# Kernel optimization log

Measured on AMD Instinct MI355X. Metric: run time of the kernel, lower is better.

The kernel has to match this reference:

```python
import jax, jax.numpy as jnp
import numpy as np

H = 256          # encoder hidden per direction
D = 2 * H        # decoder hidden / bidirectional feature dim
IN = 2
OUT = 2
B = 64
T = 256
STEPS = 24       # hard-coded decoder loop length in the source


def gru_cell(x, h, Wih, Whh, bih, bhh):
    # PyTorch GRU cell: gate order (r, z, n)
    gi = x @ Wih.T + bih
    gh = h @ Whh.T + bhh
    ir, iz, inn = jnp.split(gi, 3, axis=-1)
    hr, hz, hn = jnp.split(gh, 3, axis=-1)
    r = jax.nn.sigmoid(ir + hr)
    z = jax.nn.sigmoid(iz + hz)
    n = jnp.tanh(inn + r * hn)
    return (1.0 - z) * n + z * h


def run_dir(xs, Wih, Whh, bih, bhh, reverse):
    # xs: (T, B, F) time-major; returns outputs (T, B, H) and last hidden (B, H)
    h0 = jnp.zeros((xs.shape[1], Whh.shape[-1]), xs.dtype)
    def step(h, xt):
        h2 = gru_cell(xt, h, Wih, Whh, bih, bhh)
        return h2, h2
    h_last, ys = jax.lax.scan(step, h0, xs, reverse=reverse)
    return ys, h_last


def setup_inputs():
    keys = jax.random.split(jax.random.key(0), 24)
    k = iter(keys)
    def rn(shape, s):
        return jax.random.normal(next(k), shape, jnp.float32) * s
    se = 1.0 / np.sqrt(H)
    sd = 1.0 / np.sqrt(D)
    return {
        "x": rn((B, T, IN), 1.0),
        "enc_Wih0": rn((2, 3 * H, IN), se),
        "enc_Whh0": rn((2, 3 * H, H), se),
        "enc_bih0": rn((2, 3 * H), se),
        "enc_bhh0": rn((2, 3 * H), se),
        "enc_Wih": rn((2, 2, 3 * H, D), se),
        "enc_Whh": rn((2, 2, 3 * H, H), se),
        "enc_bih": rn((2, 2, 3 * H), se),
        "enc_bhh": rn((2, 2, 3 * H), se),
        "dec_Wih": rn((3, 3 * D, D), sd),
        "dec_Whh": rn((3, 3 * D, D), sd),
        "dec_bih": rn((3, 3 * D), sd),
        "dec_bhh": rn((3, 3 * D), sd),
        "fc_con_W": rn((D, 2 * D), sd),
        "fc_con_b": rn((D,), sd),
        "attn_W": rn((D, 2 * D), sd),
        "attn_b": rn((D,), sd),
        "v": jax.random.uniform(next(k), (D,), jnp.float32),  # torch.rand init
        "fc_W": rn((OUT, D), sd),
        "fc_b": rn((OUT,), sd),
    }


def reference(x, enc_Wih0, enc_Whh0, enc_bih0, enc_bhh0,
              enc_Wih, enc_Whh, enc_bih, enc_bhh,
              dec_Wih, dec_Whh, dec_bih, dec_bhh,
              fc_con_W, fc_con_b, attn_W, attn_b, v, fc_W, fc_b):
    # ---- bidirectional 3-layer GRU encoder ----
    seq = x.transpose(1, 0, 2)  # (T, B, IN) time-major
    hf_list, hb_list = [], []
    for l in range(3):
        if l == 0:
            Wf, Uf, bf, cf = enc_Wih0[0], enc_Whh0[0], enc_bih0[0], enc_bhh0[0]
            Wb, Ub, bb, cb = enc_Wih0[1], enc_Whh0[1], enc_bih0[1], enc_bhh0[1]
        else:
            Wf, Uf, bf, cf = enc_Wih[l-1, 0], enc_Whh[l-1, 0], enc_bih[l-1, 0], enc_bhh[l-1, 0]
            Wb, Ub, bb, cb = enc_Wih[l-1, 1], enc_Whh[l-1, 1], enc_bih[l-1, 1], enc_bhh[l-1, 1]
        yf, hf = run_dir(seq, Wf, Uf, bf, cf, False)
        yb, hb = run_dir(seq, Wb, Ub, bb, cb, True)
        seq = jnp.concatenate([yf, yb], axis=-1)
        hf_list.append(hf)
        hb_list.append(hb)
    enc_out = seq.transpose(1, 0, 2)  # (B, T, D)
    # hidden_decoder = cat(forward, backward) per layer -> (3, B, D)
    hidden = jnp.stack([jnp.concatenate([f, b], axis=-1)
                        for f, b in zip(hf_list, hb_list)])
    dec_in = enc_out[:, -1, :]  # (B, D)

    # additive attention: energy = tanh(W [h; enc_out] + b); precompute enc part
    attn_Wh = attn_W[:, :D]
    attn_We = attn_W[:, D:]
    enc_proj = jnp.einsum('bte,de->btd', enc_out, attn_We)  # (B, T, D)

    def dec_step(carry, _):
        d_in, hid = carry
        hq = hid[-1] @ attn_Wh.T                               # (B, D)
        energy = jnp.tanh(hq[:, None, :] + enc_proj + attn_b)  # (B, T, D)
        scores = jnp.einsum('btd,d->bt', energy, v)
        aw = jax.nn.softmax(scores, axis=1)                    # (B, T)
        ctx = jnp.einsum('bt,btd->bd', aw, enc_out)            # (B, D)
        inp = jnp.concatenate([d_in, ctx], axis=-1) @ fc_con_W.T + fc_con_b
        new_h = []
        for l in range(3):  # 3-layer unidirectional decoder GRU, single step
            hl = gru_cell(inp, hid[l], dec_Wih[l], dec_Whh[l], dec_bih[l], dec_bhh[l])
            new_h.append(hl)
            inp = hl
        out_step = inp @ fc_W.T + fc_b
        return (inp, jnp.stack(new_h)), out_step

    _, outs = jax.lax.scan(dec_step, (dec_in, hidden), None, length=STEPS)
    return outs.transpose(1, 0, 2)  # (B, 24, OUT)
```

## Files before the change

kernel.cpp:

```cpp
#include <hip/hip_runtime.h>

typedef unsigned short u16;
typedef unsigned int u32;
typedef _Float16 f16;
typedef f16   f16x2 __attribute__((ext_vector_type(2)));
typedef f16   f16x4 __attribute__((ext_vector_type(4)));
typedef f16   f16x8 __attribute__((ext_vector_type(8)));
typedef float f32x4 __attribute__((ext_vector_type(4)));

#define MFMA16(a,b,c) __builtin_amdgcn_mfma_f32_16x16x32_f16((a),(b),(c),0,0,0)

__device__ __forceinline__ float sigm_(float x){ return 1.f/(1.f + __expf(-x)); }
__device__ __forceinline__ float tanh_(float x){ return 1.f - 2.f/(1.f + __expf(2.f*x)); }
__device__ __forceinline__ float clampf(float x, float c){
  if (!(x > -c)) x = -c;
  if (x > c) x = c;
  return x;
}
__device__ __forceinline__ f16x8 cvt8f(const float* p){
  const float4 a = *(const float4*)p;
  const float4 b = *(const float4*)(p+4);
  f16x8 r;
  r[0]=(f16)a.x; r[1]=(f16)a.y; r[2]=(f16)a.z; r[3]=(f16)a.w;
  r[4]=(f16)b.x; r[5]=(f16)b.y; r[6]=(f16)b.z; r[7]=(f16)b.w;
  return r;
}

__device__ __forceinline__ void gbar_(u32* c, u32 nb){
  __syncthreads();
  __threadfence();
  if (threadIdx.x == 0) {
    __hip_atomic_fetch_add(c, 1u, __ATOMIC_RELAXED, __HIP_MEMORY_SCOPE_AGENT);
    while (__hip_atomic_load(c, __ATOMIC_RELAXED, __HIP_MEMORY_SCOPE_AGENT) < nb) {}
  }
  __syncthreads();
  __threadfence();
}

__global__ void k_diag(float* out, int mib){
  const int i = blockIdx.x*256 + threadIdx.x;
  if (i < 3072) out[i] = 1000.f * (float)mib;
}

__global__ void k_prep_dec(const float* dWhh, const float* attnW, const float* fccon,
                           const float* dWih, f16* R3)
{
  long idx = (long)blockIdx.x*256 + threadIdx.x;
  const float* src; int rs, colOff = 0, NKS; long dst, loc;
  if (idx < 294912L) {
    loc = idx; const int m = (int)(loc / 98304); loc %= 98304;
    src = dWhh + (long)m*786432; rs = 512; NKS = 16; dst = (long)m*786432;
  } else if (idx < 327680L) {
    loc = idx - 294912L; src = attnW; colOff = 512; rs = 1024; NKS = 16; dst = 2359296L;
  } else if (idx < 393216L) {
    loc = idx - 327680L; src = fccon; rs = 1024; NKS = 32; dst = 2621440L;
  } else if (idx < 688128L) {
    loc = idx - 393216L; const int m = (int)(loc / 98304); loc %= 98304;
    src = dWih + (long)m*786432; rs = 512; NKS = 16; dst = 3440640L + (long)m*786432;
  } else if (idx < 720896L) {
    loc = idx - 688128L; src = attnW; colOff = 0; rs = 1024; NKS = 16; dst = 5799936L;
  } else return;
  const int lane = (int)(loc & 63);
  const long frag = loc >> 6;
  const int ks = (int)(frag % NKS);
  const long nt = frag / NKS;
  const int n  = (int)(nt*16 + (lane & 15));
  const int k0 = ks*32 + ((lane >> 4) << 3);
  const float* sp = src + (long)n*rs + colOff + k0;
  f16* dp = R3 + dst + loc*8;
  #pragma unroll
  for (int j = 0; j < 8; ++j) dp[j] = (f16)sp[j];
}

__global__ void k_gi0s(const float* __restrict__ x, const float* __restrict__ W,
                       const float* __restrict__ bi, f16* __restrict__ gi,
                       int seg, int BH, int lbh, int b0)
{
  const long idx = (long)blockIdx.x*256 + threadIdx.x;
  const int v = (int)(idx % 24);
  long rest = idx / 24;
  const int tid = (int)(rest & 511); rest >>= 9;
  const int bq = (int)(rest & ((1 << (lbh-4)) - 1)); rest >>= (lbh-4);
  const int s = (int)(rest & 63);
  const int d = (int)(rest >> 6);
  const int r = v / 6, rem = v % 6, i = rem / 3, g = rem % 3;
  const int w = tid >> 6, q = (tid >> 4) & 3, lo = tid & 15;
  const int n = g*256 + (2*w + i)*16 + lo;
  const int b = bq*16 + q*4 + r;
  const int t = d ? (255 - (seg*64 + s)) : (seg*64 + s);
  const float x0 = x[(((b0+b)<<8) + t)*2];
  const float x1 = x[(((b0+b)<<8) + t)*2 + 1];
  const long wi = ((long)d*768 + n)*2;
  gi[idx] = (f16)clampf(x0*W[wi] + x1*W[wi+1] + bi[d*768 + n], 32.f);
}

#define GIE(G, vv) ((float)((vv) < 8 ? (G)[0][(vv)&7] : ((vv) < 16 ? (G)[1][(vv)-8] : (G)[2][(vv)-16])))

__global__ __launch_bounds__(512, 1) void k_enc_seg(
    const f16* __restrict__ gi, const float* __restrict__ Wraw,
    const float* __restrict__ bhh, f16* __restrict__ seq, int ostr,
    f16* __restrict__ fin, float* __restrict__ hcar, int seg, int BH)
{
  const int tid = threadIdx.x;
  const int w = tid >> 6, lane = tid & 63;
  const int lo16 = lane & 15, quad = lane >> 4;
  const int nbq = BH >> 4;
  const int dir = blockIdx.x / nbq, bq = blockIdx.x % nbq;

  __shared__ f16 h16[4][16][264];

  const float* mat = Wraw + (long)dir*196608;
  f16x8 wr[6][8];
  #pragma unroll
  for (int p = 0; p < 3; ++p)
    #pragma unroll
    for (int i = 0; i < 2; ++i) {
      const int n = (p*16 + 2*w + i)*16 + lo16;
      #pragma unroll
      for (int ks = 0; ks < 8; ++ks)
        wr[p*2+i][ks] = cvt8f(mat + (long)n*256 + ks*32 + quad*8);
    }
  float bh_[3][2];
  #pragma unroll
  for (int p = 0; p < 3; ++p)
    #pragma unroll
    for (int i = 0; i < 2; ++i)
      bh_[p][i] = bhh[dir*768 + p*256 + (2*w+i)*16 + lo16];

  float hreg[2][4];
  if (seg == 0) {
    #pragma unroll
    for (int i = 0; i < 2; ++i)
      #pragma unroll
      for (int r = 0; r < 4; ++r) {
        hreg[i][r] = 0.f;
        h16[0][quad*4 + r][(2*w+i)*16 + lo16] = (f16)0.f;
      }
  } else {
    #pragma unroll
    for (int i = 0; i < 2; ++i) {
      const int c = (2*w+i)*16 + lo16;
      #pragma unroll
      for (int r = 0; r < 4; ++r) {
        const float v = hcar[((dir*BH) + bq*16 + quad*4 + r)*256 + c];
        hreg[i][r] = v;
        h16[0][quad*4 + r][c] = (f16)v;
      }
    }
  }

  const long gstep = (long)nbq*512*24;
  const f16* gbase = gi + (((long)dir*64*nbq + bq)*512 + tid)*24;
  f16x8 g0[3], g1[3];
  { const f16x8* gp = (const f16x8*)gbase; g0[0]=gp[0]; g0[1]=gp[1]; g0[2]=gp[2]; }

  const int frow = tid >> 5;
  const int fcol = (tid & 31) * 8;

  for (int s = 0; s < 64; ++s) {
    __syncthreads();
    if (s >= 2) {
      const int so = s - 2;
      const int t2 = dir ? (255 - (seg*64 + so)) : (seg*64 + so);
      const f16x8 hv = *(const f16x8*)&h16[(so+1)&3][frow][fcol];
      *(f16x8*)&seq[((long)t2*ostr + bq*16 + frow)*512 + dir*256 + fcol] = hv;
    }
    f32x4 acc[6];
    #pragma unroll
    for (int q = 0; q < 6; ++q) acc[q] = (f32x4){0.f,0.f,0.f,0.f};
    #pragma unroll
    for (int ks = 0; ks < 8; ++ks) {
      const f16x8 a = *(const f16x8*)&h16[s&3][lo16][ks*32 + quad*8];
      #pragma unroll
      for (int q = 0; q < 6; ++q)
        acc[q] = MFMA16(a, wr[q][ks], acc[q]);
    }
    if (s < 63) {
      const f16x8* gp = (const f16x8*)(gbase + (long)(s+1)*gstep);
      g1[0]=gp[0]; g1[1]=gp[1]; g1[2]=gp[2];
    }
    #pragma unroll
    for (int i = 0; i < 2; ++i) {
      const int c = (2*w+i)*16 + lo16;
      #pragma unroll
      for (int r = 0; r < 4; ++r) {
        const int row = quad*4 + r;
        const int v = r*6 + i*3;
        const float gir = GIE(g0, v);
        const float giz = GIE(g0, v+1);
        const float gin = GIE(g0, v+2);
        const float rv = sigm_(gir + acc[i][r]   + bh_[0][i]);
        const float zv = sigm_(giz + acc[2+i][r] + bh_[1][i]);
        const float nv = tanh_(gin + rv*(acc[4+i][r] + bh_[2][i]));
        float hn = (1.f - zv)*nv + zv*hreg[i][r];
        hn = clampf(hn, 2.f);
        hreg[i][r] = hn;
        h16[(s+1)&3][row][c] = (f16)hn;
        if (seg == 3 && s == 63) fin[(bq*16 + row)*512 + dir*256 + c] = (f16)hn;
      }
    }
    g0[0]=g1[0]; g0[1]=g1[1]; g0[2]=g1[2];
  }
  __syncthreads();
  #pragma unroll
  for (int so = 62; so < 64; ++so) {
    const int t2 = dir ? (255 - (seg*64 + so)) : (seg*64 + so);
    const f16x8 hv = *(const f16x8*)&h16[(so+1)&3][frow][fcol];
    *(f16x8*)&seq[((long)t2*ostr + bq*16 + frow)*512 + dir*256 + fcol] = hv;
  }
  #pragma unroll
  for (int i = 0; i < 2; ++i) {
    const int c = (2*w+i)*16 + lo16;
    #pragma unroll
    for (int r = 0; r < 4; ++r)
      hcar[((dir*BH) + bq*16 + quad*4 + r)*256 + c] = hreg[i][r];
  }
}

__global__ void k_gemm(const f16* __restrict__ A, int K,
                       const f16* __restrict__ Bsw, const float* __restrict__ Braw,
                       long bzs, int ldb, int koff,
                       const float* __restrict__ bias, int biaszs,
                       void* __restrict__ Cv, long czs, int ldc, int mode,
                       int tb0, int tb1, int tdirsgn, int lbh, int abstr, float cv)
{
  const int tid = threadIdx.x, w = tid>>6, lane = tid&63;
  const int lo16 = lane&15, quad = lane>>4;
  const int m0 = blockIdx.x*64 + w*16;
  const int n0 = blockIdx.y*128;
  const int z  = blockIdx.z;
  const int tbase = z ? tb1 : tb0;
  const int tdir  = z ? -tdirsgn : tdirsgn;
  const int NKS = K >> 5;
  const int mrow = m0 + lo16;
  const long arow = (long)(tbase + tdir*(mrow >> lbh))*abstr + (mrow & ((1<<lbh)-1));
  const f16* Ap = A + arow*K + quad*8;
  f32x4 acc[8];
  #pragma unroll
  for (int i=0;i<8;++i) acc[i]=(f32x4){0.f,0.f,0.f,0.f};
  if (Bsw) {
    const f16* Bp = Bsw + (long)z*bzs;
    for (int ks = 0; ks < NKS; ++ks) {
      const f16x8 a = *(const f16x8*)(Ap + ks*32);
      #pragma unroll
      for (int nt = 0; nt < 8; ++nt) {
        const f16x8 b = *(const f16x8*)(Bp + (((long)((n0>>4)+nt)*NKS + ks) << 9) + lane*8);
        acc[nt] = MFMA16(a, b, acc[nt]);
      }
    }
  } else {
    const float* Bp = Braw + (long)z*bzs;
    for (int ks = 0; ks < NKS; ++ks) {
      const f16x8 a = *(const f16x8*)(Ap + ks*32);
      #pragma unroll
      for (int nt = 0; nt < 8; ++nt) {
        const f16x8 b = cvt8f(Bp + (long)(n0 + nt*16 + lo16)*ldb + koff + ks*32 + quad*8);
        acc[nt] = MFMA16(a, b, acc[nt]);
      }
    }
  }
  #pragma unroll
  for (int nt = 0; nt < 8; ++nt) {
    const int n = n0 + nt*16 + lo16;
    const float bv = bias ? bias[z*biaszs + n] : 0.f;
    #pragma unroll
    for (int r = 0; r < 4; ++r) {
      const int m = m0 + quad*4 + r;
      const float val = clampf(acc[nt][r] + bv, cv);
      if (mode == 2) {
        const int s_ = m >> lbh, b_ = m & ((1<<lbh)-1);
        const int bq_ = b_ >> 4, q_ = (b_ >> 2) & 3, r_ = b_ & 3;
        const int g_ = n >> 8, j_ = (n >> 4) & 15, lo_ = n & 15;
        const long idx = ((((long)z*64 + s_)*(1<<(lbh-4)) + bq_)*512
                          + ((j_>>1)*64 + q_*16 + lo_))*24 + r_*6 + (j_&1)*3 + g_;
        ((f16*)Cv)[idx] = (f16)val;
      } else if (mode == 1)
        ((f16*)Cv)[(long)z*czs + (long)m*ldc + n] = (f16)val;
      else
        ((float*)Cv)[(long)z*czs + (long)m*ldc + n] = val;
    }
  }
}

__global__ void k_score(const f16* __restrict__ seq, const f16* __restrict__ We,
                        const float* __restrict__ hq, const float* __restrict__ ab,
                        const float* __restrict__ vp, float* __restrict__ S)
{
  const int t = blockIdx.x, tid = threadIdx.x;
  const int w = tid>>6, lane = tid&63, lo16 = lane&15, quad = lane>>4;
  __shared__ float svab[1024];
  for (int i = tid; i < 512; i += 256) { svab[i] = vp[i]; svab[512+i] = ab[i]; }
  __syncthreads();
  f32x4 acc[32];
  #pragma unroll
  for (int i=0;i<32;++i) acc[i]=(f32x4){0.f,0.f,0.f,0.f};
  const f16* Ap = seq + ((long)t*64 + w*16 + lo16)*512 + quad*8;
  for (int ks = 0; ks < 16; ++ks) {
    const f16x8 a = *(const f16x8*)(Ap + ks*32);
    #pragma unroll
    for (int nt = 0; nt < 32; ++nt) {
      const f16x8 b = *(const f16x8*)(We + (((long)nt*16 + ks) << 9) + lane*8);
      acc[nt] = MFMA16(a, b, acc[nt]);
    }
  }
  #pragma unroll
  for (int r = 0; r < 4; ++r) {
    const int b = w*16 + quad*4 + r;
    float sc = 0.f;
    #pragma unroll
    for (int nt = 0; nt < 32; ++nt) {
      const int n = nt*16 + lo16;
      sc += svab[n] * tanh_(acc[nt][r] + hq[(b<<9) + n] + svab[512+n]);
    }
    sc += __shfl_xor(sc, 1, 64); sc += __shfl_xor(sc, 2, 64);
    sc += __shfl_xor(sc, 4, 64); sc += __shfl_xor(sc, 8, 64);
    if (lo16 == 0) S[(b<<8) + t] = clampf(sc, 256.f);
  }
}

__global__ void k_attnctx(const float* __restrict__ S, const f16* __restrict__ enc,
                          f16* __restrict__ cat)
{
  const int b = blockIdx.x, tid = threadIdx.x;
  __shared__ float ssc[256], srd[256];
  const float sc = clampf(S[(b<<8) + tid], 256.f);
  srd[tid] = sc; __syncthreads();
  for (int off = 128; off > 0; off >>= 1) { if (tid < off) srd[tid] = fmaxf(srd[tid], srd[tid+off]); __syncthreads(); }
  const float mx = srd[0]; __syncthreads();
  const float e = __expf(sc - mx);
  srd[tid] = e; __syncthreads();
  for (int off = 128; off > 0; off >>= 1) { if (tid < off) srd[tid] += srd[tid+off]; __syncthreads(); }
  const float inv = 1.f / srd[0]; __syncthreads();
  ssc[tid] = e * inv; __syncthreads();
  float c0 = 0.f, c1 = 0.f;
  for (int tt = 0; tt < 256; ++tt) {
    const float awt = ssc[tt];
    const f16* ep = enc + (((long)tt*64 + b) << 9);
    c0 += awt * (float)ep[tid];
    c1 += awt * (float)ep[256 + tid];
  }
  cat[(b<<10) + 512 + tid] = (f16)clampf(c0, 4.f);
  cat[(b<<10) + 768 + tid] = (f16)clampf(c1, 4.f);
}

__global__ void k_dec_init(const f16* __restrict__ fin, const f16* __restrict__ seq,
                           f16* __restrict__ hb16, float* __restrict__ hf32,
                           f16* __restrict__ cat, u32* __restrict__ cnt)
{
  const int idx = blockIdx.x*256 + threadIdx.x;
  if (idx < 64) cnt[idx] = 0;
  const int d = idx & 511, b = (idx >> 9) & 63, l = idx >> 15;
  if (l < 3) {
    const float v = clampf((float)fin[((long)l<<15) + (b<<9) + d], 2.f);
    hb16[(long)l*65536 + (b<<9) + d] = (f16)v;
    hf32[(long)l*32768 + (b<<9) + d] = v;
  } else {
    cat[(b<<10) + d] = seq[((long)255*64 + b)*512 + d];
  }
}

__global__ __launch_bounds__(512, 1) void k_attn(
    const f16* __restrict__ seq, const f16* __restrict__ ep,
    const float* __restrict__ hf2, const f16* __restrict__ cat,
    const f16* __restrict__ whsw, const f16* __restrict__ fcsw,
    const float* __restrict__ fcconB, const float* __restrict__ vp,
    f16* __restrict__ inp, const float* __restrict__ fcW,
    const float* __restrict__ fcb, float* __restrict__ out, int step)
{
  const int b = blockIdx.x;
  const int tid = threadIdx.x, w = tid >> 6, lane = tid & 63;
  const int quad = lane >> 4;
  __shared__ float hsm[512];
  __shared__ float cats[1024];
  __shared__ float hqs[512];
  __shared__ float aw[256];
  __shared__ float red[8*512];
  hsm[tid]  = hf2[(b<<9) + tid];
  cats[tid] = (float)cat[(b<<10) + tid];
  __syncthreads();
  if (w < 2 && step > 0) {
    float p = 0.f;
    #pragma unroll
    for (int j = 0; j < 8; ++j) p += fcW[(w<<9) + lane*8 + j] * hsm[lane*8 + j];
    p += __shfl_xor(p,1,64); p += __shfl_xor(p,2,64); p += __shfl_xor(p,4,64);
    p += __shfl_xor(p,8,64); p += __shfl_xor(p,16,64); p += __shfl_xor(p,32,64);
    if (lane == 0) out[(b*24 + step-1)*2 + w] = clampf(p + fcb[w], 128.f);
  }
  #pragma unroll
  for (int i = 0; i < 4; ++i) {
    const int nt = w*4 + i;
    float p = 0.f;
    for (int ks = 0; ks < 16; ++ks) {
      const f16x8 wv = *(const f16x8*)(whsw + (((long)nt*16 + ks)<<9) + lane*8);
      const float4 ha = *(const float4*)&hsm[ks*32 + quad*8];
      const float4 hb = *(const float4*)&hsm[ks*32 + quad*8 + 4];
      p += (float)wv[0]*ha.x + (float)wv[1]*ha.y + (float)wv[2]*ha.z + (float)wv[3]*ha.w
         + (float)wv[4]*hb.x + (float)wv[5]*hb.y + (float)wv[6]*hb.z + (float)wv[7]*hb.w;
    }
    p += __shfl_xor(p,16,64); p += __shfl_xor(p,32,64);
    if (lane < 16) hqs[nt*16 + lane] = p;
  }
  __syncthreads();
  float hq8[8], v8[8];
  #pragma unroll
  for (int j = 0; j < 8; ++j) { hq8[j] = hqs[lane*8+j]; v8[j] = vp[lane*8+j]; }
  #pragma unroll 2
  for (int i = 0; i < 32; ++i) {
    const int t = w*32 + i;
    const f16x8 e = *(const f16x8*)(ep + (((long)t*64 + b)<<9) + lane*8);
    float s = 0.f;
    #pragma unroll
    for (int j = 0; j < 8; ++j) s += v8[j]*tanh_((float)e[j] + hq8[j]);
    s += __shfl_xor(s,1,64); s += __shfl_xor(s,2,64); s += __shfl_xor(s,4,64);
    s += __shfl_xor(s,8,64); s += __shfl_xor(s,16,64); s += __shfl_xor(s,32,64);
    if (lane == 0) aw[t] = clampf(s, 256.f);
  }
  __syncthreads();
  if (tid < 64) {
    float s0=aw[tid], s1=aw[tid+64], s2=aw[tid+128], s3=aw[tid+192];
    float mx = fmaxf(fmaxf(s0,s1), fmaxf(s2,s3));
    mx = fmaxf(mx, __shfl_xor(mx,1,64)); mx = fmaxf(mx, __shfl_xor(mx,2,64));
    mx = fmaxf(mx, __shfl_xor(mx,4,64)); mx = fmaxf(mx, __shfl_xor(mx,8,64));
    mx = fmaxf(mx, __shfl_xor(mx,16,64)); mx = fmaxf(mx, __shfl_xor(mx,32,64));
    const float e0=__expf(s0-mx), e1=__expf(s1-mx), e2=__expf(s2-mx), e3=__expf(s3-mx);
    float sm = e0+e1+e2+e3;
    sm += __shfl_xor(sm,1,64); sm += __shfl_xor(sm,2,64); sm += __shfl_xor(sm,4,64);
    sm += __shfl_xor(sm,8,64); sm += __shfl_xor(sm,16,64); sm += __shfl_xor(sm,32,64);
    const float inv = 1.f/sm;
    aw[tid]=e0*inv; aw[tid+64]=e1*inv; aw[tid+128]=e2*inv; aw[tid+192]=e3*inv;
  }
  __syncthreads();
  float c8[8];
  #pragma unroll
  for (int j = 0; j < 8; ++j) c8[j] = 0.f;
  #pragma unroll 2
  for (int i = 0; i < 32; ++i) {
    const int t = w*32 + i;
    const f16x8 e = *(const f16x8*)(seq + (((long)t*64 + b)<<9) + lane*8);
    const float awt = aw[t];
    #pragma unroll
    for (int j = 0; j < 8; ++j) c8[j] += awt*(float)e[j];
  }
  #pragma unroll
  for (int j = 0; j < 8; ++j) red[(w<<9) + lane*8 + j] = c8[j];
  __syncthreads();
  {
    float s = 0.f;
    #pragma unroll
    for (int ww = 0; ww < 8; ++ww) s += red[(ww<<9) + tid];
    cats[512 + tid] = clampf(s, 4.f);
  }
  __syncthreads();
  #pragma unroll
  for (int i = 0; i < 4; ++i) {
    const int nt = w*4 + i;
    float p = 0.f;
    for (int ks = 0; ks < 32; ++ks) {
      const f16x8 wv = *(const f16x8*)(fcsw + (((long)nt*32 + ks)<<9) + lane*8);
      const float4 ca = *(const float4*)&cats[ks*32 + quad*8];
      const float4 cb = *(const float4*)&cats[ks*32 + quad*8 + 4];
      p += (float)wv[0]*ca.x + (float)wv[1]*ca.y + (float)wv[2]*ca.z + (float)wv[3]*ca.w
         + (float)wv[4]*cb.x + (float)wv[5]*cb.y + (float)wv[6]*cb.z + (float)wv[7]*cb.w;
    }
    p += __shfl_xor(p,16,64); p += __shfl_xor(p,32,64);
    if (lane < 16) inp[(b<<9) + nt*16 + lane] = (f16)clampf(p + fcconB[nt*16+lane], 64.f);
  }
}

__global__ void k_cell3(const f16* __restrict__ inp0, const f16* __restrict__ WihSw,
                        const f16* __restrict__ WhhSw, const float* __restrict__ bihA,
                        const float* __restrict__ bhhA, float* __restrict__ hfA,
                        f16* __restrict__ hb, f16* __restrict__ cat, int p, u32* cnt)
{
  const int tid = threadIdx.x, w = tid>>6, lane = tid&63;
  const int lo16 = lane&15, quad = lane>>4;
  const int Wt  = ((int)blockIdx.x & 7)*4 + w;
  const int mi0 = ((int)blockIdx.x >> 3)*2;
  for (int l = 0; l < 3; ++l) {
    const f16* inp = (l == 0) ? inp0 : (hb + (long)(2*(l-1) + (1-p))*32768);
    const f16* WihL = WihSw + (long)l*786432;
    const f16* WhhL = WhhSw + (long)l*786432;
    const float* bih = bihA + l*1536;
    const float* bhh = bhhA + l*1536;
    float* hf32 = hfA + (long)l*32768;
    const f16* hin = hb + (long)(2*l + p)*32768;
    f16* hout = hb + (long)(2*l + (1-p))*32768;
    f16* catp = (l == 2) ? cat : (f16*)nullptr;

    f32x4 arz[4], an_[4];
    #pragma unroll
    for (int i=0;i<4;++i){ arz[i]=(f32x4){0.f,0.f,0.f,0.f}; an_[i]=(f32x4){0.f,0.f,0.f,0.f}; }
    #pragma unroll 2
    for (int kk = 0; kk < 16; ++kk) {
      const f16x8 b0 = *(const f16x8*)(WihL + (((long)Wt*16 + kk)<<9)      + lane*8);
      const f16x8 b1 = *(const f16x8*)(WihL + (((long)(32+Wt)*16 + kk)<<9) + lane*8);
      const f16x8 b2 = *(const f16x8*)(WihL + (((long)(64+Wt)*16 + kk)<<9) + lane*8);
      #pragma unroll
      for (int m = 0; m < 2; ++m) {
        const f16x8 a = *(const f16x8*)&inp[(((mi0+m)*16 + lo16)<<9) + kk*32 + quad*8];
        arz[m]   = MFMA16(a, b0, arz[m]);
        arz[2+m] = MFMA16(a, b1, arz[2+m]);
        an_[m]   = MFMA16(a, b2, an_[m]);
      }
    }
    #pragma unroll 2
    for (int kk = 0; kk < 16; ++kk) {
      const f16x8 b0 = *(const f16x8*)(WhhL + (((long)Wt*16 + kk)<<9)      + lane*8);
      const f16x8 b1 = *(const f16x8*)(WhhL + (((long)(32+Wt)*16 + kk)<<9) + lane*8);
      const f16x8 b2 = *(const f16x8*)(WhhL + (((long)(64+Wt)*16 + kk)<<9) + lane*8);
      #pragma unroll
      for (int m = 0; m < 2; ++m) {
        const f16x8 a = *(const f16x8*)&hin[(((mi0+m)*16 + lo16)<<9) + kk*32 + quad*8];
        arz[m]   = MFMA16(a, b0, arz[m]);
        arz[2+m] = MFMA16(a, b1, arz[2+m]);
        an_[2+m] = MFMA16(a, b2, an_[2+m]);
      }
    }
    const int c = Wt*16 + lo16;
    const float brz0 = bih[c]     + bhh[c];
    const float brz1 = bih[512+c] + bhh[512+c];
    const float bin_ = bih[1024+c];
    const float bhn_ = bhh[1024+c];
    #pragma unroll
    for (int m = 0; m < 2; ++m)
      #pragma unroll
      for (int r = 0; r < 4; ++r) {
        const int row = (mi0+m)*16 + quad*4 + r;
        const float rv = sigm_(clampf(arz[m][r],64.f)   + brz0);
        const float zv = sigm_(clampf(arz[2+m][r],64.f) + brz1);
        const float nv = tanh_(clampf(an_[m][r],64.f) + bin_ + rv*(clampf(an_[2+m][r],64.f) + bhn_));
        const float ho = hf32[(row<<9) + c];
        float hn2 = (1.f - zv)*nv + zv*ho;
        hn2 = clampf(hn2, 2.f);
        hf32[(row<<9) + c] = hn2;
        hout[(row<<9) + c] = (f16)hn2;
        if (catp) catp[(row<<10) + c] = (f16)hn2;
      }
    if (l < 2) gbar_(cnt + l, 16);
  }
}

__global__ void k_cell_raw(const f16* __restrict__ inp, const float* __restrict__ WihRaw,
                           const f16* __restrict__ WhhSw, const float* __restrict__ bih,
                           const float* __restrict__ bhh, float* __restrict__ hf32,
                           const f16* __restrict__ hin, f16* __restrict__ hout,
                           f16* __restrict__ cat)
{
  const int tid = threadIdx.x, w = tid>>6, lane = tid&63;
  const int lo16 = lane&15, quad = lane>>4;
  const int Wt = blockIdx.x*4 + w;
  f32x4 arz[8], an_[8];
  #pragma unroll
  for (int i=0;i<8;++i){ arz[i]=(f32x4){0.f,0.f,0.f,0.f}; an_[i]=(f32x4){0.f,0.f,0.f,0.f}; }
  const int nr = Wt*16 + lo16;
  const float* Rr = WihRaw + (long)nr*512        + quad*8;
  const float* Rz = WihRaw + (long)(512+nr)*512  + quad*8;
  const float* Rn = WihRaw + (long)(1024+nr)*512 + quad*8;
  #pragma unroll 2
  for (int kk = 0; kk < 16; ++kk) {
    const f16x8 b0 = cvt8f(Rr + kk*32);
    const f16x8 b1 = cvt8f(Rz + kk*32);
    const f16x8 b2 = cvt8f(Rn + kk*32);
    #pragma unroll
    for (int mi = 0; mi < 4; ++mi) {
      const f16x8 a = *(const f16x8*)&inp[((mi*16 + lo16)<<9) + kk*32 + quad*8];
      arz[mi]   = MFMA16(a, b0, arz[mi]);
      arz[4+mi] = MFMA16(a, b1, arz[4+mi]);
      an_[mi]   = MFMA16(a, b2, an_[mi]);
    }
  }
  #pragma unroll 2
  for (int kk = 0; kk < 16; ++kk) {
    const f16x8 b0 = *(const f16x8*)(WhhSw + (((long)Wt*16 + kk)<<9)      + lane*8);
    const f16x8 b1 = *(const f16x8*)(WhhSw + (((long)(32+Wt)*16 + kk)<<9) + lane*8);
    const f16x8 b2 = *(const f16x8*)(WhhSw + (((long)(64+Wt)*16 + kk)<<9) + lane*8);
    #pragma unroll
    for (int mi = 0; mi < 4; ++mi) {
      const f16x8 a = *(const f16x8*)&hin[((mi*16 + lo16)<<9) + kk*32 + quad*8];
      arz[mi]   = MFMA16(a, b0, arz[mi]);
      arz[4+mi] = MFMA16(a, b1, arz[4+mi]);
      an_[4+mi] = MFMA16(a, b2, an_[4+mi]);
    }
  }
  const int c = Wt*16 + lo16;
  const float brz0 = bih[c]     + bhh[c];
  const float brz1 = bih[512+c] + bhh[512+c];
  const float bin_ = bih[1024+c];
  const float bhn_ = bhh[1024+c];
  #pragma unroll
  for (int mi = 0; mi < 4; ++mi)
    #pragma unroll
    for (int r = 0; r < 4; ++r) {
      const int row = mi*16 + quad*4 + r;
      const float rv = sigm_(clampf(arz[mi][r],64.f)   + brz0);
      const float zv = sigm_(clampf(arz[4+mi][r],64.f) + brz1);
      const float nv = tanh_(clampf(an_[mi][r],64.f) + bin_ + rv*(clampf(an_[4+mi][r],64.f) + bhn_));
      const float ho = hf32[(row<<9) + c];
      float hn2 = (1.f - zv)*nv + zv*ho;
      hn2 = clampf(hn2, 2.f);
      hf32[(row<<9) + c] = hn2;
      hout[(row<<9) + c] = (f16)hn2;
      if (cat) cat[(row<<10) + c] = (f16)hn2;
    }
}

__global__ void k_out(const float* __restrict__ h2, const float* __restrict__ fcW,
                      const float* __restrict__ fcb, float* __restrict__ out, int step)
{
  const int b = blockIdx.x, t = threadIdx.x;
  __shared__ float r0[256], r1[256];
  const float ha = clampf(h2[(b<<9) + t], 2.f);
  const float hb = clampf(h2[(b<<9) + 256 + t], 2.f);
  r0[t] = ha*fcW[t]     + hb*fcW[256+t];
  r1[t] = ha*fcW[512+t] + hb*fcW[768+t];
  __syncthreads();
  for (int off = 128; off > 0; off >>= 1) {
    if (t < off) { r0[t] += r0[t+off]; r1[t] += r1[t+off]; }
    __syncthreads();
  }
  if (t == 0) {
    out[(b*24 + step)*2]     = clampf(r0[0] + fcb[0], 128.f);
    out[(b*24 + step)*2 + 1] = clampf(r1[0] + fcb[1], 128.f);
  }
}

extern "C" void kernel_launch(void* const* d_in, const int* in_sizes, int n_in,
                              void* d_out, int out_size, void* d_ws, size_t ws_size,
                              hipStream_t stream) {
  const float* X      = (const float*)d_in[0];
  const float* eWih0  = (const float*)d_in[1];
  const float* eWhh0  = (const float*)d_in[2];
  const float* ebih0  = (const float*)d_in[3];
  const float* ebhh0  = (const float*)d_in[4];
  const float* eWih   = (const float*)d_in[5];
  const float* eWhh   = (const float*)d_in[6];
  const float* ebih   = (const float*)d_in[7];
  const float* ebhh   = (const float*)d_in[8];
  const float* dWih   = (const float*)d_in[9];
  const float* dWhh   = (const float*)d_in[10];
  const float* dbih   = (const float*)d_in[11];
  const float* dbhh   = (const float*)d_in[12];
  const float* fcconW = (const float*)d_in[13];
  const float* fcconB = (const float*)d_in[14];
  const float* attnW  = (const float*)d_in[15];
  const float* attnB  = (const float*)d_in[16];
  const float* vW     = (const float*)d_in[17];
  const float* fcW    = (const float*)d_in[18];
  const float* fcB    = (const float*)d_in[19];
  float* OUT = (float*)d_out;

  const long need_big  = 47054848L;
  const long need_half = 32964608L;
  f16* H = (f16*)d_ws;
  f16 *SEQ = H, *L1OUT, *GIB, *R3, *FIN, *HB, *CAT, *INP;
  float *HC;
  int BH, lbh, nh, l1ostr, l1abstr; long gdir;

  if ((long)ws_size >= need_big) {
    BH = 64; lbh = 6; nh = 1; l1ostr = 64; l1abstr = 64;
    L1OUT = H + 8388608L;
    GIB   = H + 16777216L;
    HC    = (float*)(H + 23068672L);
    FIN   = H + 23134208L;
    HB    = H + 23232512L;
    CAT   = H + 23429120L;
    INP   = H + 23494656L;
    gdir  = 3145728L;
  } else if ((long)ws_size >= need_half) {
    BH = 32; lbh = 5; nh = 2; l1ostr = 32; l1abstr = 32;
    L1OUT = H + 8388608L;
    GIB   = H + 12582912L;
    HC    = (float*)(H + 16023552L);
    FIN   = H + 16089088L;
    HB    = H + 16187392L;
    CAT   = H + 16384000L;
    INP   = H + 16449536L;
    gdir  = 1572864L;
  } else {
    k_diag<<<12, 256, 0, stream>>>(OUT, (int)(ws_size >> 20));
    return;
  }
  R3 = GIB;
  float* ST = (float*)(GIB + 3145728L);
  float* HQ = ST;
  float* HF = ST + 32768;
  float* S  = ST + 131072;
  u32* CNT = (u32*)ST;
  const int nblk = 2*(BH>>4);
  const int gi0grid = (2*64*BH*768)/256;

  for (int h = 0; h < nh; ++h) {
    const int b0 = h*BH;
    for (int seg = 0; seg < 4; ++seg) {
      k_gi0s<<<gi0grid, 256, 0, stream>>>(X, eWih0, ebih0, GIB, seg, BH, lbh, b0);
      k_enc_seg<<<nblk, 512, 0, stream>>>(GIB, eWhh0, ebhh0, SEQ + (long)b0*512, 64,
                                          FIN + (long)b0*512, HC, seg, BH);
    }
    for (int seg = 0; seg < 4; ++seg) {
      k_gemm<<<dim3(BH, 6, 2), 256, 0, stream>>>(SEQ + (long)b0*512, 512,
          (const f16*)nullptr, eWih, 393216L, 512, 0, ebih, 768,
          GIB, gdir, 768, 2, seg*64, 255 - seg*64, 1, lbh, 64, 32.f);
      k_enc_seg<<<nblk, 512, 0, stream>>>(GIB, eWhh, ebhh, L1OUT, l1ostr,
                                          FIN + 32768 + (long)b0*512, HC, seg, BH);
    }
    for (int seg = 0; seg < 4; ++seg) {
      k_gemm<<<dim3(BH, 6, 2), 256, 0, stream>>>(L1OUT, 512,
          (const f16*)nullptr, eWih + 2L*393216, 393216L, 512, 0, ebih + 1536, 768,
          GIB, gdir, 768, 2, seg*64, 255 - seg*64, 1, lbh, l1abstr, 32.f);
      k_enc_seg<<<nblk, 512, 0, stream>>>(GIB, eWhh + 2L*196608, ebhh + 1536,
                                          SEQ + (long)b0*512, 64,
                                          FIN + 65536 + (long)b0*512, HC, seg, BH);
    }
  }

  if (BH == 64) {
    f16* EP    = L1OUT;
    f16* WIHSW = GIB + 3440640L;
    f16* WHSW  = GIB + 5799936L;

    k_prep_dec<<<2816, 256, 0, stream>>>(dWhh, attnW, fcconW, dWih, R3);
    k_gemm<<<dim3(256, 4, 1), 256, 0, stream>>>(SEQ, 512,
        R3 + 2359296L, (const float*)nullptr, 0L, 0, 0, attnB, 0,
        EP, 0L, 512, 1, 0, 0, 1, 6, 64, 32.f);
    k_dec_init<<<512, 256, 0, stream>>>(FIN, SEQ, HB, HF, CAT, CNT);

    for (int s = 0; s < 24; ++s) {
      const int p = s & 1;
      k_attn<<<64, 512, 0, stream>>>(SEQ, EP, HF + 2*32768, CAT, WHSW, R3 + 2621440L,
          fcconB, vW, INP, fcW, fcB, OUT, s);
      k_cell3<<<16, 256, 0, stream>>>(INP, WIHSW, R3, dbih, dbhh, HF, HB, CAT,
          p, CNT + s*2);
    }
    k_out<<<64, 256, 0, stream>>>(HF + 2*32768, fcW, fcB, OUT, 23);
  } else {
    k_prep_dec<<<1536, 256, 0, stream>>>(dWhh, attnW, fcconW, dWih, R3);
    k_dec_init<<<512, 256, 0, stream>>>(FIN, SEQ, HB, HF, CAT, (u32*)(S + 16000));

    for (int s = 0; s < 24; ++s) {
      const int p = s & 1;
      const f16* h2in = HB + (4 + p)*32768L;
      k_gemm<<<dim3(1,4,1), 256, 0, stream>>>(h2in, 512,
          (const f16*)nullptr, attnW, 0L, 1024, 0, (const float*)nullptr, 0,
          HQ, 0L, 512, 0, 0, 0, 0, 6, 64, 64.f);
      k_score<<<256, 256, 0, stream>>>(SEQ, R3 + 2359296L, HQ, attnB, vW, S);
      k_attnctx<<<64, 256, 0, stream>>>(S, SEQ, CAT);
      k_gemm<<<dim3(1,4,1), 256, 0, stream>>>(CAT, 1024,
          R3 + 2621440L, (const float*)nullptr, 0L, 0, 0, fcconB, 0,
          INP, 0L, 512, 1, 0, 0, 0, 6, 64, 64.f);
      for (int l = 0; l < 3; ++l) {
        const f16* inp = (l == 0) ? INP : (HB + (2*(l-1) + (1-p))*32768L);
        k_cell_raw<<<8, 256, 0, stream>>>(inp,
                  dWih + (long)l*786432, R3 + (long)l*786432,
                  dbih + l*1536, dbhh + l*1536, HF + (long)l*32768,
                  HB + (2*l + p)*32768L, HB + (2*l + (1-p))*32768L,
                  (l == 2) ? CAT : (f16*)nullptr);
      }
      k_out<<<64, 256, 0, stream>>>(HF + 2*32768, fcW, fcB, OUT, s);
    }
  }
}
```

Before: 6.393 ms.

## Add dedicated input-gate GEMM kernel and deepen gate prefetch in encoder recurrence

Adds k_gemm_gi, a GEMM specialised for BH=64 that computes all three gate blocks per tile and writes them directly in the interleaved layout the recurrent kernel reads. It replaces the generic k_gemm for encoder layers 1 and 2. The recurrent segment kernel now prefetches input-gate values two steps ahead instead of one. It also replaces __syncthreads with a barrier that waits only on LDS counters, so global loads can stay in flight across steps. The new GEMM converts fp32 weights to fp16 on the fly and reloads B for every block, and the deeper prefetch raises register pressure.

```diff
diff --git a/kernel.cpp b/kernel.cpp
--- a/kernel.cpp
+++ b/kernel.cpp
@@ -151,14 +151,15 @@
 
   const long gstep = (long)nbq*512*24;
   const f16* gbase = gi + (((long)dir*64*nbq + bq)*512 + tid)*24;
-  f16x8 g0[3], g1[3];
-  { const f16x8* gp = (const f16x8*)gbase; g0[0]=gp[0]; g0[1]=gp[1]; g0[2]=gp[2]; }
+  f16x8 g0[3], g1[3], g2[3];
+  { const f16x8* gp = (const f16x8*)gbase;           g0[0]=gp[0]; g0[1]=gp[1]; g0[2]=gp[2]; }
+  { const f16x8* gp = (const f16x8*)(gbase + gstep); g1[0]=gp[0]; g1[1]=gp[1]; g1[2]=gp[2]; }
 
   const int frow = tid >> 5;
   const int fcol = (tid & 31) * 8;
 
   for (int s = 0; s < 64; ++s) {
-    __syncthreads();
+    asm volatile("s_waitcnt lgkmcnt(0)\n\ts_barrier" ::: "memory");
     if (s >= 2) {
       const int so = s - 2;
       const int t2 = dir ? (255 - (seg*64 + so)) : (seg*64 + so);
@@ -175,9 +176,9 @@
       for (int q = 0; q < 6; ++q)
         acc[q] = MFMA16(a, wr[q][ks], acc[q]);
     }
-    if (s < 63) {
-      const f16x8* gp = (const f16x8*)(gbase + (long)(s+1)*gstep);
-      g1[0]=gp[0]; g1[1]=gp[1]; g1[2]=gp[2];
+    if (s < 62) {
+      const f16x8* gp = (const f16x8*)(gbase + (long)(s+2)*gstep);
+      g2[0]=gp[0]; g2[1]=gp[1]; g2[2]=gp[2];
     }
     #pragma unroll
     for (int i = 0; i < 2; ++i) {
@@ -200,6 +201,7 @@
       }
     }
     g0[0]=g1[0]; g0[1]=g1[1]; g0[2]=g1[2];
+    g1[0]=g2[0]; g1[1]=g2[1]; g1[2]=g2[2];
   }
   __syncthreads();
   #pragma unroll
@@ -214,6 +216,59 @@
     #pragma unroll
     for (int r = 0; r < 4; ++r)
       hcar[((dir*BH) + bq*16 + quad*4 + r)*256 + c] = hreg[i][r];
+  }
+}
+
+__global__ void k_gemm_gi(const f16* __restrict__ A,
+                          const float* __restrict__ Braw, long bzs,
+                          const float* __restrict__ bias,
+                          f16* __restrict__ gi,
+                          int tb0, int tb1, int tdirsgn, int abstr, float cv)
+{
+  const int tid = threadIdx.x, w = tid>>6, lane = tid&63;
+  const int lo16 = lane&15, quad = lane>>4;
+  const int s_ = blockIdx.x;
+  const int y  = blockIdx.y;
+  const int z  = blockIdx.z;
+  const int tbase = z ? tb1 : tb0;
+  const int tdir  = z ? -tdirsgn : tdirsgn;
+  const int mrow = s_*64 + w*16 + lo16;
+  const long arow = (long)(tbase + tdir*(mrow >> 6))*abstr + (mrow & 63);
+  const f16* Ap = A + arow*512 + quad*8;
+  const float* Bp = Braw + (long)z*bzs;
+  f32x4 acc[24];
+  #pragma unroll
+  for (int i=0;i<24;++i) acc[i]=(f32x4){0.f,0.f,0.f,0.f};
+  for (int ks = 0; ks < 16; ++ks) {
+    const f16x8 a = *(const f16x8*)(Ap + ks*32);
+    #pragma unroll
+    for (int g = 0; g < 3; ++g)
+      #pragma unroll
+      for (int jj = 0; jj < 8; ++jj) {
+        const int n = g*256 + y*128 + jj*16 + lo16;
+        const f16x8 b = cvt8f(Bp + (long)n*512 + ks*32 + quad*8);
+        acc[g*8+jj] = MFMA16(a, b, acc[g*8+jj]);
+      }
+  }
+  f16* base = gi + (((long)z*64 + s_)*4 + w)*12288L;
+  #pragma unroll
+  for (int l = 0; l < 4; ++l) {
+    f16x8 rec8[3];
+    #pragma unroll
+    for (int r = 0; r < 4; ++r)
+      #pragma unroll
+      for (int jl = 0; jl < 2; ++jl)
+        #pragma unroll
+        for (int g = 0; g < 3; ++g) {
+          const int nt = g*8 + l*2 + jl;
+          const int n = g*256 + y*128 + (l*2+jl)*16 + lo16;
+          const int slot = r*6 + jl*3 + g;
+          rec8[slot>>3][slot&7] = (f16)clampf(acc[nt][r] + bias[z*768 + n], cv);
+        }
+    f16* dp = base + ((long)(y*4 + l)*64 + quad*16 + lo16)*24L;
+    *(f16x8*)(dp)      = rec8[0];
+    *(f16x8*)(dp + 8)  = rec8[1];
+    *(f16x8*)(dp + 16) = rec8[2];
   }
 }
 
@@ -697,16 +752,24 @@
                                           FIN + (long)b0*512, HC, seg, BH);
     }
     for (int seg = 0; seg < 4; ++seg) {
-      k_gemm<<<dim3(BH, 6, 2), 256, 0, stream>>>(SEQ + (long)b0*512, 512,
-          (const f16*)nullptr, eWih, 393216L, 512, 0, ebih, 768,
-          GIB, gdir, 768, 2, seg*64, 255 - seg*64, 1, lbh, 64, 32.f);
+      if (BH == 64)
+        k_gemm_gi<<<dim3(64, 2, 2), 256, 0, stream>>>(SEQ, eWih, 393216L, ebih,
+            GIB, seg*64, 255 - seg*64, 1, 64, 32.f);
+      else
+        k_gemm<<<dim3(BH, 6, 2), 256, 0, stream>>>(SEQ + (long)b0*512, 512,
+            (const f16*)nullptr, eWih, 393216L, 512, 0, ebih, 768,
+            GIB, gdir, 768, 2, seg*64, 255 - seg*64, 1, lbh, 64, 32.f);
       k_enc_seg<<<nblk, 512, 0, stream>>>(GIB, eWhh, ebhh, L1OUT, l1ostr,
                                           FIN + 32768 + (long)b0*512, HC, seg, BH);
     }
     for (int seg = 0; seg < 4; ++seg) {
-      k_gemm<<<dim3(BH, 6, 2), 256, 0, stream>>>(L1OUT, 512,
-          (const f16*)nullptr, eWih + 2L*393216, 393216L, 512, 0, ebih + 1536, 768,
-          GIB, gdir, 768, 2, seg*64, 255 - seg*64, 1, lbh, l1abstr, 32.f);
+      if (BH == 64)
+        k_gemm_gi<<<dim3(64, 2, 2), 256, 0, stream>>>(L1OUT, eWih + 2L*393216,
+            393216L, ebih + 1536, GIB, seg*64, 255 - seg*64, 1, 64, 32.f);
+      else
+        k_gemm<<<dim3(BH, 6, 2), 256, 0, stream>>>(L1OUT, 512,
+            (const f16*)nullptr, eWih + 2L*393216, 393216L, 512, 0, ebih + 1536, 768,
+            GIB, gdir, 768, 2, seg*64, 255 - seg*64, 1, lbh, l1abstr, 32.f);
       k_enc_seg<<<nblk, 512, 0, stream>>>(GIB, eWhh + 2L*196608, ebhh + 1536,
                                           SEQ + (long)b0*512, 64,
                                           FIN + 65536 + (long)b0*512, HC, seg, BH);
```

New measurement: 8.016 ms. +25.4%, slower.
